# Kernel tuning notes

Hardware: AMD Instinct MI355X
Metric: run time of the kernel (lower is better)

Reference implementation:

```python
import jax, jax.numpy as jnp
import numpy as np

EPS_BN = 1e-5


def setup_inputs() -> dict:
    key = jax.random.key(0)
    ks = jax.random.split(key, 6)
    n, L, D, G = 10000, 256, 32, 3
    return {
        "pop": jax.random.normal(ks[0], (n, L), dtype=jnp.float32),
        "conv_w": jax.random.normal(ks[1], (D, 1, 1), dtype=jnp.float32) * 0.1,
        "conv_b": jnp.zeros((D,), dtype=jnp.float32),
        "bn_gamma": jnp.ones((D,), dtype=jnp.float32),
        "bn_beta": jnp.zeros((D,), dtype=jnp.float32),
        "gcn_ws": jax.random.normal(ks[2], (G, D, D), dtype=jnp.float32) * (1.0 / np.sqrt(D)),
        "gcn_bs": jnp.zeros((G, D), dtype=jnp.float32),
        "out_w": jax.random.normal(ks[3], (D, 3), dtype=jnp.float32) * (1.0 / np.sqrt(D)),
        "out_b": jnp.zeros((3,), dtype=jnp.float32),
        "k": 32,
    }


def _knn_edges(x, k):
    # x: [n, d]. PyG knn_graph(loop=False): edges (neighbor j -> center i).
    n = x.shape[0]
    sq = jnp.sum(x * x, axis=-1)  # [n]
    d2 = sq[:, None] + sq[None, :] - 2.0 * (x @ x.T)  # [n, n]
    idx = jnp.arange(n)
    d2 = d2.at[idx, idx].set(jnp.inf)  # exclude self (loop=False)
    _, nbr = jax.lax.top_k(-d2, k)  # [n, k] nearest neighbors of each node
    src = nbr.reshape(-1)                       # sources (neighbors)
    dst = jnp.repeat(idx, k)                    # targets (centers)
    return src, dst


def _gcn(x, W, b, src, dst, deg_isqrt):
    # GCNConv with self-loops already folded into (src, dst) and deg.
    h = x @ W  # [n, D_out]
    norm = deg_isqrt[src] * deg_isqrt[dst]  # [E]
    msg = h[src] * norm[:, None]
    agg = jax.ops.segment_sum(msg, dst, num_segments=x.shape[0])
    return agg + b


def reference(pop, conv_w, conv_b, bn_gamma, bn_beta, gcn_ws, gcn_bs, out_w, out_b, k):
    n, L = pop.shape
    # --- stem: Conv1d(1, D, kernel=1) -> y[n, c, l] = pop[n, l] * w[c] + b[c]
    w = conv_w[:, 0, 0]  # [D]
    y = pop[:, None, :] * w[None, :, None] + conv_b[None, :, None]  # [n, D, L]
    # --- BatchNorm1d (training mode: batch stats over (N, L), biased var)
    mean = jnp.mean(y, axis=(0, 2))
    var = jnp.mean(jnp.square(y - mean[None, :, None]), axis=(0, 2))
    y = (y - mean[None, :, None]) * (bn_gamma / jnp.sqrt(var + EPS_BN))[None, :, None] + bn_beta[None, :, None]
    y = jax.nn.silu(y)
    # --- adaptive avg pool to length 1 -> mean over L
    x = jnp.mean(y, axis=-1)  # [n, D]
    # --- knn graph on pooled features
    src, dst = _knn_edges(x, k)
    # add self loops (GCNConv default)
    idx = jnp.arange(n)
    src_f = jnp.concatenate([src, idx])
    dst_f = jnp.concatenate([dst, idx])
    deg = jax.ops.segment_sum(jnp.ones_like(dst_f, dtype=x.dtype), dst_f, num_segments=n)
    deg_isqrt = jnp.where(deg > 0, 1.0 / jnp.sqrt(deg), 0.0)
    # --- stacked GCNs
    for i in range(gcn_ws.shape[0]):
        x = _gcn(x, gcn_ws[i], gcn_bs[i], src_f, dst_f, deg_isqrt)
        x = jax.nn.silu(x)
    x = _gcn(x, out_w, out_b, src_f, dst_f, deg_isqrt)  # [n, 3]
    return jax.nn.softmax(x, axis=-1)
```

## Files before the change

### kernel.cpp

```cpp
#include <hip/hip_runtime.h>
#include <math.h>

#define N_NODES 10000
#define NPAD    10016
#define L_LEN   256
#define D_DIM   32
#define K_NBR   32
#define NTOT    (N_NODES * L_LEN)
#define EPS_BN  1e-5f
#define QB      3
#define BT      1024
#define SD      3

typedef unsigned int uint4_ev __attribute__((ext_vector_type(4)));

__device__ __forceinline__ float silu_f(float x) {
    return x / (1.0f + expf(-x));
}

__global__ void stats_kernel(const float* __restrict__ pop, float* __restrict__ stats) {
    __shared__ float s1[256], s2[256];
    int t = threadIdx.x;
    float a = 0.f, b = 0.f;
    for (int idx = blockIdx.x * 256 + t; idx < NTOT; idx += gridDim.x * 256) {
        float v = pop[idx];
        a += v; b += v * v;
    }
    s1[t] = a; s2[t] = b;
    __syncthreads();
    for (int s = 128; s > 0; s >>= 1) {
        if (t < s) { s1[t] += s1[t + s]; s2[t] += s2[t + s]; }
        __syncthreads();
    }
    if (t == 0) { atomicAdd(&stats[0], s1[0]); atomicAdd(&stats[1], s2[0]); }
}

__global__ void feat_kernel(const float* __restrict__ pop,
                            const float* __restrict__ conv_w,
                            const float* __restrict__ conv_b,
                            const float* __restrict__ gamma,
                            const float* __restrict__ beta,
                            const float* __restrict__ stats,
                            float* __restrict__ X,
                            float* __restrict__ XT,
                            float* __restrict__ SQ) {
    __shared__ float row[L_LEN];
    __shared__ float part[256];
    int i = blockIdx.x;
    int t = threadIdx.x;
    row[t] = pop[i * L_LEN + t];
    __syncthreads();
    int d = t & 31, g = t >> 5;
    float M  = stats[0] * (1.0f / NTOT);
    float Vc = stats[1] * (1.0f / NTOT) - M * M;
    float w = conv_w[d], b = conv_b[d];
    float mean = fmaf(w, M, b);
    float var  = w * w * Vc;
    float sc = gamma[d] / sqrtf(var + EPS_BN);
    float bt = beta[d];
    float acc = 0.f;
    int l0 = g * 32;
    #pragma unroll
    for (int l = 0; l < 32; ++l) {
        float y = fmaf(row[l0 + l], w, b);
        float z = fmaf(y - mean, sc, bt);
        acc += silu_f(z);
    }
    part[t] = acc;
    __syncthreads();
    if (t < 32) {
        float s = 0.f;
        #pragma unroll
        for (int gg = 0; gg < 8; ++gg) s += part[gg * 32 + t];
        float xv = s * (1.0f / L_LEN);
        X[i * D_DIM + t] = xv;
        XT[t * N_NODES + i] = xv;
        part[t] = xv;
    }
    __syncthreads();
    if (t == 0) {
        float sq = 0.f;
        #pragma unroll
        for (int dd = 0; dd < 32; ++dd) sq += part[dd] * part[dd];
        SQ[i] = sq;
    }
}

__global__ __launch_bounds__(BT) void knn3_kernel(const float* __restrict__ X,
                                                  const float* __restrict__ XT,
                                                  const float* __restrict__ SQ,
                                                  int* __restrict__ NBR) {
    extern __shared__ unsigned int keys[];
    __shared__ float qv[QB][D_DIM];
    __shared__ float sqq[QB];
    __shared__ unsigned int hist[256];
    __shared__ unsigned int sprefix;
    __shared__ int swant, scnt, slast;

    int t = threadIdx.x;
    int q0 = blockIdx.x * QB;

    if (t < QB * D_DIM) {
        int q = t >> 5, d = t & 31;
        int gq = q0 + q;
        qv[q][d] = (gq < N_NODES) ? X[gq * D_DIM + d] : 0.f;
    }
    if (t < QB) sqq[t] = (q0 + t < N_NODES) ? SQ[q0 + t] : 0.f;
    __syncthreads();

    float acc[QB][SD * 4];
    #pragma unroll
    for (int q = 0; q < QB; ++q)
        #pragma unroll
        for (int s = 0; s < SD * 4; ++s) acc[q][s] = 0.f;

    #pragma unroll 2
    for (int d = 0; d < D_DIM; ++d) {
        float qd0 = qv[0][d], qd1 = qv[1][d], qd2 = qv[2][d];
        const float4* xr4 = (const float4*)(XT + d * N_NODES);
        #pragma unroll
        for (int s = 0; s < SD; ++s) {
            int i4 = t + s * BT;
            float4 xv = make_float4(0.f, 0.f, 0.f, 0.f);
            if (i4 < N_NODES / 4) xv = xr4[i4];
            acc[0][s * 4 + 0] = fmaf(qd0, xv.x, acc[0][s * 4 + 0]);
            acc[0][s * 4 + 1] = fmaf(qd0, xv.y, acc[0][s * 4 + 1]);
            acc[0][s * 4 + 2] = fmaf(qd0, xv.z, acc[0][s * 4 + 2]);
            acc[0][s * 4 + 3] = fmaf(qd0, xv.w, acc[0][s * 4 + 3]);
            acc[1][s * 4 + 0] = fmaf(qd1, xv.x, acc[1][s * 4 + 0]);
            acc[1][s * 4 + 1] = fmaf(qd1, xv.y, acc[1][s * 4 + 1]);
            acc[1][s * 4 + 2] = fmaf(qd1, xv.z, acc[1][s * 4 + 2]);
            acc[1][s * 4 + 3] = fmaf(qd1, xv.w, acc[1][s * 4 + 3]);
            acc[2][s * 4 + 0] = fmaf(qd2, xv.x, acc[2][s * 4 + 0]);
            acc[2][s * 4 + 1] = fmaf(qd2, xv.y, acc[2][s * 4 + 1]);
            acc[2][s * 4 + 2] = fmaf(qd2, xv.z, acc[2][s * 4 + 2]);
            acc[2][s * 4 + 3] = fmaf(qd2, xv.w, acc[2][s * 4 + 3]);
        }
    }

    const float4* sq4p = (const float4*)SQ;
    #pragma unroll
    for (int s = 0; s < SD; ++s) {
        int i4 = t + s * BT;
        int j4 = 4 * i4;
        if (j4 < NPAD) {
            float4 sj = make_float4(0.f, 0.f, 0.f, 0.f);
            if (i4 < N_NODES / 4) sj = sq4p[i4];
            float sjv[4] = { sj.x, sj.y, sj.z, sj.w };
            #pragma unroll
            for (int q = 0; q < QB; ++q) {
                int gq = q0 + q;
                unsigned int kk[4];
                #pragma unroll
                for (int jj = 0; jj < 4; ++jj) {
                    int j = j4 + jj;
                    unsigned int kv = 0xFFFFFFFFu;
                    if (j < N_NODES && gq < N_NODES && j != gq) {
                        float d2 = (sqq[q] + sjv[jj]) - 2.0f * acc[q][s * 4 + jj];
                        unsigned int u = __float_as_uint(d2);
                        u ^= (u & 0x80000000u) ? 0xFFFFFFFFu : 0x80000000u;
                        kv = u;
                    }
                    kk[jj] = kv;
                }
                uint4_ev w = { kk[0], kk[1], kk[2], kk[3] };
                *(uint4_ev*)&keys[q * NPAD + j4] = w;
            }
        }
    }
    __syncthreads();

    for (int q = 0; q < QB; ++q) {
        int gq = q0 + q;
        if (gq >= N_NODES) break;
        unsigned int* kq = keys + q * NPAD;
        if (t == 0) { sprefix = 0u; swant = K_NBR; scnt = 0; }
        __syncthreads();

        for (int r = 0; r < 4; ++r) {
            if (t < 256) hist[t] = 0u;
            __syncthreads();
            unsigned int pfxR = sprefix;
            int wantR = swant;
            int shift = 24 - 8 * r;
            for (int s = 0; s < 10; ++s) {
                int j = t + s * BT;
                if (j < NPAD) {
                    unsigned int u = kq[j];
                    bool match = (r == 0) || ((u >> (shift + 8)) == pfxR);
                    if (match) atomicAdd(&hist[(u >> shift) & 255u], 1u);
                }
            }
            __syncthreads();
            if (t < 64) {
                int lane = t;
                unsigned int c[4];
                unsigned int gsum = 0u;
                #pragma unroll
                for (int i = 0; i < 4; ++i) { c[i] = hist[4 * lane + i]; gsum += c[i]; }
                unsigned int x = gsum;
                #pragma unroll
                for (int off = 1; off < 64; off <<= 1) {
                    unsigned int y = (unsigned int)__shfl_up((int)x, off);
                    if (lane >= off) x += y;
                }
                unsigned int e = x - gsum;
                #pragma unroll
                for (int i = 0; i < 4; ++i) {
                    if (e < (unsigned int)wantR && (unsigned int)wantR <= e + c[i]) {
                        swant = wantR - (int)e;
                        sprefix = (pfxR << 8) | (unsigned int)(4 * lane + i);
                    }
                    e += c[i];
                }
            }
            __syncthreads();
        }

        unsigned int kth = sprefix;
        int wantEq = swant;
        for (int s = 0; s < 10; ++s) {
            int j = t + s * BT;
            if (j < N_NODES && kq[j] < kth) {
                int p = atomicAdd(&scnt, 1);
                NBR[gq * K_NBR + p] = j;
            }
        }
        __syncthreads();
        int base = scnt;
        int last = -1;
        for (int e = 0; e < wantEq; ++e) {
            unsigned int best = 0xFFFFFFFFu;
            for (int s = 0; s < 10; ++s) {
                int j = t + s * BT;
                if (j < N_NODES && kq[j] == kth && j > last)
                    best = best < (unsigned int)j ? best : (unsigned int)j;
            }
            #pragma unroll
            for (int off = 32; off > 0; off >>= 1) {
                unsigned int o = (unsigned int)__shfl_xor((int)best, off);
                best = best < o ? best : o;
            }
            if ((t & 63) == 0) hist[t >> 6] = best;
            __syncthreads();
            if (t == 0) {
                unsigned int m = 0xFFFFFFFFu;
                #pragma unroll
                for (int w = 0; w < 16; ++w) m = m < hist[w] ? m : hist[w];
                NBR[gq * K_NBR + base + e] = (int)m;
                slast = (int)m;
            }
            __syncthreads();
            last = slast;
            __syncthreads();
        }
    }
}

__global__ void gcn_mm(const float* __restrict__ X, const float* __restrict__ W,
                       float* __restrict__ H) {
    __shared__ float Ws[D_DIM * D_DIM];
    int t = threadIdx.x;
    #pragma unroll
    for (int q = 0; q < 4; ++q) Ws[q * 256 + t] = W[q * 256 + t];
    __syncthreads();
    int i = blockIdx.x * 8 + (t >> 5);
    int d = t & 31;
    const float* xr = X + i * D_DIM;
    float acc = 0.f;
    #pragma unroll
    for (int m = 0; m < D_DIM; ++m)
        acc = fmaf(xr[m], Ws[m * D_DIM + d], acc);
    H[i * D_DIM + d] = acc;
}

__global__ void gcn_agg(const float* __restrict__ H, const int* __restrict__ NBR,
                        const float* __restrict__ bias, float* __restrict__ Xout,
                        int do_silu) {
    __shared__ int nb[256];
    int t = threadIdx.x;
    int i0 = blockIdx.x * 8;
    nb[t] = NBR[i0 * K_NBR + t];
    __syncthreads();
    int i = i0 + (t >> 5);
    int d = t & 31;
    float acc = H[i * D_DIM + d];
    int base = (t >> 5) * K_NBR;
    #pragma unroll 8
    for (int s = 0; s < K_NBR; ++s) {
        int j = nb[base + s];
        acc += H[j * D_DIM + d];
    }
    const float r = 1.0f / sqrtf(33.0f);
    const float nrm = r * r;
    float v = fmaf(acc, nrm, bias[d]);
    if (do_silu) v = silu_f(v);
    Xout[i * D_DIM + d] = v;
}

__global__ void out_mm(const float* __restrict__ X, const float* __restrict__ W,
                       float* __restrict__ HOUT) {
    __shared__ float Ws[D_DIM * 3];
    int t = threadIdx.x;
    if (t < D_DIM * 3) Ws[t] = W[t];
    __syncthreads();
    int i = blockIdx.x * 256 + t;
    if (i >= N_NODES) return;
    float a0 = 0.f, a1 = 0.f, a2 = 0.f;
    #pragma unroll
    for (int m = 0; m < D_DIM; ++m) {
        float xv = X[i * D_DIM + m];
        a0 = fmaf(xv, Ws[m * 3 + 0], a0);
        a1 = fmaf(xv, Ws[m * 3 + 1], a1);
        a2 = fmaf(xv, Ws[m * 3 + 2], a2);
    }
    HOUT[i * 3 + 0] = a0; HOUT[i * 3 + 1] = a1; HOUT[i * 3 + 2] = a2;
}

__global__ void final_kernel(const float* __restrict__ HOUT, const int* __restrict__ NBR,
                             const float* __restrict__ out_b, float* __restrict__ out) {
    int i = blockIdx.x * 256 + threadIdx.x;
    if (i >= N_NODES) return;
    float a0 = HOUT[i * 3 + 0], a1 = HOUT[i * 3 + 1], a2 = HOUT[i * 3 + 2];
    for (int s = 0; s < K_NBR; ++s) {
        int j = NBR[i * K_NBR + s];
        a0 += HOUT[j * 3 + 0];
        a1 += HOUT[j * 3 + 1];
        a2 += HOUT[j * 3 + 2];
    }
    const float r = 1.0f / sqrtf(33.0f);
    const float nrm = r * r;
    float v0 = fmaf(a0, nrm, out_b[0]);
    float v1 = fmaf(a1, nrm, out_b[1]);
    float v2 = fmaf(a2, nrm, out_b[2]);
    float m = fmaxf(v0, fmaxf(v1, v2));
    float e0 = expf(v0 - m), e1 = expf(v1 - m), e2 = expf(v2 - m);
    float inv = 1.0f / (e0 + e1 + e2);
    out[i * 3 + 0] = e0 * inv;
    out[i * 3 + 1] = e1 * inv;
    out[i * 3 + 2] = e2 * inv;
}

extern "C" void kernel_launch(void* const* d_in, const int* in_sizes, int n_in,
                              void* d_out, int out_size, void* d_ws, size_t ws_size,
                              hipStream_t stream) {
    const float* pop    = (const float*)d_in[0];
    const float* conv_w = (const float*)d_in[1];
    const float* conv_b = (const float*)d_in[2];
    const float* gamma  = (const float*)d_in[3];
    const float* beta   = (const float*)d_in[4];
    const float* gcn_ws = (const float*)d_in[5];
    const float* gcn_bs = (const float*)d_in[6];
    const float* out_w  = (const float*)d_in[7];
    const float* out_b  = (const float*)d_in[8];

    char* ws = (char*)d_ws;
    const size_t o_stats = 0;
    const size_t o_X     = 256;
    const size_t o_XT    = o_X + 1280000;
    const size_t o_SQ    = o_XT + 1280000;
    const size_t o_H     = o_SQ + 40192;
    const size_t o_NBR   = o_H + 1280000;
    const size_t o_HOUT  = o_NBR + 1280000;

    float* stats = (float*)(ws + o_stats);
    float* X     = (float*)(ws + o_X);
    float* XT    = (float*)(ws + o_XT);
    float* SQ    = (float*)(ws + o_SQ);
    float* H     = (float*)(ws + o_H);
    int*   NBR   = (int*)  (ws + o_NBR);
    float* HOUT  = (float*)(ws + o_HOUT);
    float* out   = (float*)d_out;

    (void)hipMemsetAsync(stats, 0, 2 * sizeof(float), stream);
    stats_kernel<<<512, 256, 0, stream>>>(pop, stats);
    feat_kernel<<<N_NODES, 256, 0, stream>>>(pop, conv_w, conv_b, gamma, beta, stats, X, XT, SQ);

    const int nqb = (N_NODES + QB - 1) / QB;
    const size_t keys_bytes = (size_t)QB * NPAD * 4;
    knn3_kernel<<<nqb, BT, keys_bytes, stream>>>(X, XT, SQ, NBR);

    for (int l = 0; l < 3; ++l) {
        gcn_mm<<<N_NODES / 8, 256, 0, stream>>>(X, gcn_ws + l * D_DIM * D_DIM, H);
        gcn_agg<<<N_NODES / 8, 256, 0, stream>>>(H, NBR, gcn_bs + l * D_DIM, X, 1);
    }
    out_mm<<<(N_NODES + 255) / 256, 256, 0, stream>>>(X, out_w, HOUT);
    final_kernel<<<(N_NODES + 255) / 256, 256, 0, stream>>>(HOUT, NBR, out_b, out);
}
```

Baseline: 766.5 us.

## Parallelize kNN selection across queries and fuse GCN aggregate-then-matmul kernels

New measurement: 948.9 us. +23.8%, slower.

```diff
diff --git a/kernel.cpp b/kernel.cpp
--- a/kernel.cpp
+++ b/kernel.cpp
@@ -93,17 +93,20 @@
     extern __shared__ unsigned int keys[];
     __shared__ float qv[QB][D_DIM];
     __shared__ float sqq[QB];
-    __shared__ unsigned int hist[256];
-    __shared__ unsigned int sprefix;
-    __shared__ int swant, scnt, slast;
+    __shared__ unsigned int whist[16][256];
+    __shared__ unsigned int wmin[16], wmax[16];
+    __shared__ unsigned int gkmin[QB], gkmax[QB], gkth[QB];
+    __shared__ int gwant[QB], gcnt[QB];
 
     int t = threadIdx.x;
+    int lane = t & 63;
+    int w = t >> 6;
     int q0 = blockIdx.x * QB;
 
     if (t < QB * D_DIM) {
         int q = t >> 5, d = t & 31;
-        int gq = q0 + q;
-        qv[q][d] = (gq < N_NODES) ? X[gq * D_DIM + d] : 0.f;
+        int gq_ = q0 + q;
+        qv[q][d] = (gq_ < N_NODES) ? X[gq_ * D_DIM + d] : 0.f;
     }
     if (t < QB) sqq[t] = (q0 + t < N_NODES) ? SQ[q0 + t] : 0.f;
     __syncthreads();
@@ -149,13 +152,13 @@
             float sjv[4] = { sj.x, sj.y, sj.z, sj.w };
             #pragma unroll
             for (int q = 0; q < QB; ++q) {
-                int gq = q0 + q;
+                int gq_ = q0 + q;
                 unsigned int kk[4];
                 #pragma unroll
                 for (int jj = 0; jj < 4; ++jj) {
                     int j = j4 + jj;
                     unsigned int kv = 0xFFFFFFFFu;
-                    if (j < N_NODES && gq < N_NODES && j != gq) {
+                    if (j < N_NODES && gq_ < N_NODES && j != gq_) {
                         float d2 = (sqq[q] + sjv[jj]) - 2.0f * acc[q][s * 4 + jj];
                         unsigned int u = __float_as_uint(d2);
                         u ^= (u & 0x80000000u) ? 0xFFFFFFFFu : 0x80000000u;
@@ -163,182 +166,178 @@
                     }
                     kk[jj] = kv;
                 }
-                uint4_ev w = { kk[0], kk[1], kk[2], kk[3] };
-                *(uint4_ev*)&keys[q * NPAD + j4] = w;
-            }
-        }
-    }
-    __syncthreads();
-
-    for (int q = 0; q < QB; ++q) {
-        int gq = q0 + q;
-        if (gq >= N_NODES) break;
-        unsigned int* kq = keys + q * NPAD;
-        if (t == 0) { sprefix = 0u; swant = K_NBR; scnt = 0; }
+                uint4_ev wv = { kk[0], kk[1], kk[2], kk[3] };
+                *(uint4_ev*)&keys[q * NPAD + j4] = wv;
+            }
+        }
+    }
+    __syncthreads();
+
+    int g     = (w >= 10) ? 2 : (w >= 5 ? 1 : 0);
+    int wbase = (g == 2) ? 10 : g * 5;
+    int gsz   = (g == 2) ? 6 : 5;
+    int lt    = (w - wbase) * 64 + lane;
+    int GT    = gsz * 64;
+    unsigned int* kq = keys + g * NPAD;
+    int gq = q0 + g;
+
+    unsigned int mn = 0xFFFFFFFFu, mx = 0u;
+    for (int j = lt; j < NPAD; j += GT) {
+        unsigned int u = kq[j];
+        mn = mn < u ? mn : u;
+        if (u != 0xFFFFFFFFu) mx = mx > u ? mx : u;
+    }
+    #pragma unroll
+    for (int off = 32; off > 0; off >>= 1) {
+        unsigned int a = (unsigned int)__shfl_xor((int)mn, off);
+        unsigned int b = (unsigned int)__shfl_xor((int)mx, off);
+        mn = mn < a ? mn : a;
+        mx = mx > b ? mx : b;
+    }
+    if (lane == 0) { wmin[w] = mn; wmax[w] = mx; }
+    __syncthreads();
+    if (t < QB) {
+        int b0 = (t == 2) ? 10 : t * 5;
+        int bs = (t == 2) ? 6 : 5;
+        unsigned int m0 = 0xFFFFFFFFu, m1 = 0u;
+        for (int k = 0; k < bs; ++k) {
+            m0 = m0 < wmin[b0 + k] ? m0 : wmin[b0 + k];
+            m1 = m1 > wmax[b0 + k] ? m1 : wmax[b0 + k];
+        }
+        gkmin[t] = m0; gkmax[t] = m1;
+        gkth[t] = m0; gwant[t] = K_NBR; gcnt[t] = 0;
+    }
+    __syncthreads();
+
+    for (int shift = 24; shift >= 0; shift -= 8) {
+        unsigned int gdiff = gkmin[g] ^ gkmax[g];
+        bool skip = (gdiff >> shift) == 0;
+        if (!skip) {
+            #pragma unroll
+            for (int b = lane; b < 256; b += 64) whist[w][b] = 0u;
+            unsigned int kth = gkth[g];
+            int sh8 = shift + 8;
+            for (int j = lt; j < NPAD; j += GT) {
+                unsigned int u = kq[j];
+                if (((unsigned long long)u >> sh8) == ((unsigned long long)kth >> sh8))
+                    atomicAdd(&whist[w][(u >> shift) & 255u], 1u);
+            }
+        }
         __syncthreads();
-
-        for (int r = 0; r < 4; ++r) {
-            if (t < 256) hist[t] = 0u;
-            __syncthreads();
-            unsigned int pfxR = sprefix;
-            int wantR = swant;
-            int shift = 24 - 8 * r;
-            for (int s = 0; s < 10; ++s) {
-                int j = t + s * BT;
-                if (j < NPAD) {
-                    unsigned int u = kq[j];
-                    bool match = (r == 0) || ((u >> (shift + 8)) == pfxR);
-                    if (match) atomicAdd(&hist[(u >> shift) & 255u], 1u);
+        if (!skip && w == wbase) {
+            int want = gwant[g];
+            unsigned int kth = gkth[g];
+            unsigned int c[4]; unsigned int gsum = 0u;
+            #pragma unroll
+            for (int i = 0; i < 4; ++i) {
+                unsigned int tot = 0u; int b = 4 * lane + i;
+                for (int k = 0; k < gsz; ++k) tot += whist[wbase + k][b];
+                c[i] = tot; gsum += tot;
+            }
+            unsigned int x = gsum;
+            #pragma unroll
+            for (int off = 1; off < 64; off <<= 1) {
+                unsigned int y = (unsigned int)__shfl_up((int)x, off);
+                if (lane >= off) x += y;
+            }
+            unsigned int e = x - gsum;
+            #pragma unroll
+            for (int i = 0; i < 4; ++i) {
+                if (e < (unsigned int)want && (unsigned int)want <= e + c[i]) {
+                    gwant[g] = want - (int)e;
+                    gkth[g] = (kth & ~(255u << shift)) |
+                              ((unsigned int)(4 * lane + i) << shift);
                 }
-            }
-            __syncthreads();
-            if (t < 64) {
-                int lane = t;
-                unsigned int c[4];
-                unsigned int gsum = 0u;
+                e += c[i];
+            }
+        }
+        __syncthreads();
+    }
+
+    unsigned int kth = gkth[g];
+    int wantEq = gwant[g];
+    int baseSlot = K_NBR - wantEq;
+    if (gq < N_NODES) {
+        for (int j = lt; j < NPAD; j += GT) {
+            if (kq[j] < kth) {
+                int p = atomicAdd(&gcnt[g], 1);
+                NBR[gq * K_NBR + p] = j;
+            }
+        }
+        if (w == wbase) {
+            int last = -1;
+            for (int e = 0; e < wantEq; ++e) {
+                unsigned int best = 0xFFFFFFFFu;
+                for (int j = lane; j < NPAD; j += 64) {
+                    if (kq[j] == kth && j > last && (unsigned int)j < best)
+                        best = (unsigned int)j;
+                }
                 #pragma unroll
-                for (int i = 0; i < 4; ++i) { c[i] = hist[4 * lane + i]; gsum += c[i]; }
-                unsigned int x = gsum;
-                #pragma unroll
-                for (int off = 1; off < 64; off <<= 1) {
-                    unsigned int y = (unsigned int)__shfl_up((int)x, off);
-                    if (lane >= off) x += y;
+                for (int off = 32; off > 0; off >>= 1) {
+                    unsigned int o = (unsigned int)__shfl_xor((int)best, off);
+                    best = best < o ? best : o;
                 }
-                unsigned int e = x - gsum;
-                #pragma unroll
-                for (int i = 0; i < 4; ++i) {
-                    if (e < (unsigned int)wantR && (unsigned int)wantR <= e + c[i]) {
-                        swant = wantR - (int)e;
-                        sprefix = (pfxR << 8) | (unsigned int)(4 * lane + i);
-                    }
-                    e += c[i];
-                }
-            }
-            __syncthreads();
-        }
-
-        unsigned int kth = sprefix;
-        int wantEq = swant;
-        for (int s = 0; s < 10; ++s) {
-            int j = t + s * BT;
-            if (j < N_NODES && kq[j] < kth) {
-                int p = atomicAdd(&scnt, 1);
-                NBR[gq * K_NBR + p] = j;
-            }
-        }
-        __syncthreads();
-        int base = scnt;
-        int last = -1;
-        for (int e = 0; e < wantEq; ++e) {
-            unsigned int best = 0xFFFFFFFFu;
-            for (int s = 0; s < 10; ++s) {
-                int j = t + s * BT;
-                if (j < N_NODES && kq[j] == kth && j > last)
-                    best = best < (unsigned int)j ? best : (unsigned int)j;
-            }
-            #pragma unroll
-            for (int off = 32; off > 0; off >>= 1) {
-                unsigned int o = (unsigned int)__shfl_xor((int)best, off);
-                best = best < o ? best : o;
-            }
-            if ((t & 63) == 0) hist[t >> 6] = best;
-            __syncthreads();
-            if (t == 0) {
-                unsigned int m = 0xFFFFFFFFu;
-                #pragma unroll
-                for (int w = 0; w < 16; ++w) m = m < hist[w] ? m : hist[w];
-                NBR[gq * K_NBR + base + e] = (int)m;
-                slast = (int)m;
-            }
-            __syncthreads();
-            last = slast;
-            __syncthreads();
-        }
-    }
-}
-
-__global__ void gcn_mm(const float* __restrict__ X, const float* __restrict__ W,
-                       float* __restrict__ H) {
+                if (lane == 0) NBR[gq * K_NBR + baseSlot + e] = (int)best;
+                last = (int)best;
+            }
+        }
+    }
+}
+
+__global__ void gcn_fused(const float* __restrict__ Xin, const int* __restrict__ NBR,
+                          const float* __restrict__ W, const float* __restrict__ bias,
+                          float* __restrict__ Xout) {
     __shared__ float Ws[D_DIM * D_DIM];
-    int t = threadIdx.x;
+    __shared__ float sAgg[8][D_DIM];
+    __shared__ int nb[8][K_NBR];
+    int t = threadIdx.x, g = t >> 5, d = t & 31;
     #pragma unroll
     for (int q = 0; q < 4; ++q) Ws[q * 256 + t] = W[q * 256 + t];
-    __syncthreads();
-    int i = blockIdx.x * 8 + (t >> 5);
-    int d = t & 31;
-    const float* xr = X + i * D_DIM;
+    int i = blockIdx.x * 8 + g;
+    nb[g][d] = NBR[i * K_NBR + d];
+    __syncthreads();
+    float s = Xin[i * D_DIM + d];
+    #pragma unroll 8
+    for (int e = 0; e < K_NBR; ++e) s += Xin[nb[g][e] * D_DIM + d];
+    sAgg[g][d] = s;
+    __syncthreads();
     float acc = 0.f;
     #pragma unroll
     for (int m = 0; m < D_DIM; ++m)
-        acc = fmaf(xr[m], Ws[m * D_DIM + d], acc);
-    H[i * D_DIM + d] = acc;
-}
-
-__global__ void gcn_agg(const float* __restrict__ H, const int* __restrict__ NBR,
-                        const float* __restrict__ bias, float* __restrict__ Xout,
-                        int do_silu) {
-    __shared__ int nb[256];
-    int t = threadIdx.x;
-    int i0 = blockIdx.x * 8;
-    nb[t] = NBR[i0 * K_NBR + t];
-    __syncthreads();
-    int i = i0 + (t >> 5);
-    int d = t & 31;
-    float acc = H[i * D_DIM + d];
-    int base = (t >> 5) * K_NBR;
+        acc = fmaf(sAgg[g][m], Ws[m * D_DIM + d], acc);
+    float v = fmaf(acc, 1.0f / 33.0f, bias[d]);
+    Xout[i * D_DIM + d] = silu_f(v);
+}
+
+__global__ void out_final(const float* __restrict__ Xin, const int* __restrict__ NBR,
+                          const float* __restrict__ Wout, const float* __restrict__ out_b,
+                          float* __restrict__ out) {
+    __shared__ float Ws[D_DIM * 3];
+    __shared__ float sAgg[8][D_DIM];
+    __shared__ int nb[8][K_NBR];
+    int t = threadIdx.x, g = t >> 5, d = t & 31;
+    if (t < D_DIM * 3) Ws[t] = Wout[t];
+    int i = blockIdx.x * 8 + g;
+    nb[g][d] = NBR[i * K_NBR + d];
+    __syncthreads();
+    float s = Xin[i * D_DIM + d];
     #pragma unroll 8
-    for (int s = 0; s < K_NBR; ++s) {
-        int j = nb[base + s];
-        acc += H[j * D_DIM + d];
-    }
-    const float r = 1.0f / sqrtf(33.0f);
-    const float nrm = r * r;
-    float v = fmaf(acc, nrm, bias[d]);
-    if (do_silu) v = silu_f(v);
-    Xout[i * D_DIM + d] = v;
-}
-
-__global__ void out_mm(const float* __restrict__ X, const float* __restrict__ W,
-                       float* __restrict__ HOUT) {
-    __shared__ float Ws[D_DIM * 3];
-    int t = threadIdx.x;
-    if (t < D_DIM * 3) Ws[t] = W[t];
-    __syncthreads();
-    int i = blockIdx.x * 256 + t;
-    if (i >= N_NODES) return;
-    float a0 = 0.f, a1 = 0.f, a2 = 0.f;
-    #pragma unroll
-    for (int m = 0; m < D_DIM; ++m) {
-        float xv = X[i * D_DIM + m];
-        a0 = fmaf(xv, Ws[m * 3 + 0], a0);
-        a1 = fmaf(xv, Ws[m * 3 + 1], a1);
-        a2 = fmaf(xv, Ws[m * 3 + 2], a2);
-    }
-    HOUT[i * 3 + 0] = a0; HOUT[i * 3 + 1] = a1; HOUT[i * 3 + 2] = a2;
-}
-
-__global__ void final_kernel(const float* __restrict__ HOUT, const int* __restrict__ NBR,
-                             const float* __restrict__ out_b, float* __restrict__ out) {
-    int i = blockIdx.x * 256 + threadIdx.x;
-    if (i >= N_NODES) return;
-    float a0 = HOUT[i * 3 + 0], a1 = HOUT[i * 3 + 1], a2 = HOUT[i * 3 + 2];
-    for (int s = 0; s < K_NBR; ++s) {
-        int j = NBR[i * K_NBR + s];
-        a0 += HOUT[j * 3 + 0];
-        a1 += HOUT[j * 3 + 1];
-        a2 += HOUT[j * 3 + 2];
-    }
-    const float r = 1.0f / sqrtf(33.0f);
-    const float nrm = r * r;
-    float v0 = fmaf(a0, nrm, out_b[0]);
-    float v1 = fmaf(a1, nrm, out_b[1]);
-    float v2 = fmaf(a2, nrm, out_b[2]);
-    float m = fmaxf(v0, fmaxf(v1, v2));
-    float e0 = expf(v0 - m), e1 = expf(v1 - m), e2 = expf(v2 - m);
-    float inv = 1.0f / (e0 + e1 + e2);
-    out[i * 3 + 0] = e0 * inv;
-    out[i * 3 + 1] = e1 * inv;
-    out[i * 3 + 2] = e2 * inv;
+    for (int e = 0; e < K_NBR; ++e) s += Xin[nb[g][e] * D_DIM + d];
+    sAgg[g][d] = s;
+    __syncthreads();
+    if (d < 3) {
+        float v[3];
+        #pragma unroll
+        for (int c = 0; c < 3; ++c) {
+            float a = 0.f;
+            #pragma unroll
+            for (int m = 0; m < D_DIM; ++m) a = fmaf(sAgg[g][m], Ws[m * 3 + c], a);
+            v[c] = fmaf(a, 1.0f / 33.0f, out_b[c]);
+        }
+        float mx = fmaxf(v[0], fmaxf(v[1], v[2]));
+        float e0 = expf(v[0] - mx), e1 = expf(v[1] - mx), e2 = expf(v[2] - mx);
+        out[i * 3 + d] = expf(v[d] - mx) / (e0 + e1 + e2);
+    }
 }
 
 extern "C" void kernel_launch(void* const* d_in, const int* in_sizes, int n_in,
@@ -361,7 +360,6 @@
     const size_t o_SQ    = o_XT + 1280000;
     const size_t o_H     = o_SQ + 40192;
     const size_t o_NBR   = o_H + 1280000;
-    const size_t o_HOUT  = o_NBR + 1280000;
 
     float* stats = (float*)(ws + o_stats);
     float* X     = (float*)(ws + o_X);
@@ -369,7 +367,6 @@
     float* SQ    = (float*)(ws + o_SQ);
     float* H     = (float*)(ws + o_H);
     int*   NBR   = (int*)  (ws + o_NBR);
-    float* HOUT  = (float*)(ws + o_HOUT);
     float* out   = (float*)d_out;
 
     (void)hipMemsetAsync(stats, 0, 2 * sizeof(float), stream);
@@ -380,10 +377,8 @@
     const size_t keys_bytes = (size_t)QB * NPAD * 4;
     knn3_kernel<<<nqb, BT, keys_bytes, stream>>>(X, XT, SQ, NBR);
 
-    for (int l = 0; l < 3; ++l) {
-        gcn_mm<<<N_NODES / 8, 256, 0, stream>>>(X, gcn_ws + l * D_DIM * D_DIM, H);
-        gcn_agg<<<N_NODES / 8, 256, 0, stream>>>(H, NBR, gcn_bs + l * D_DIM, X, 1);
-    }
-    out_mm<<<(N_NODES + 255) / 256, 256, 0, stream>>>(X, out_w, HOUT);
-    final_kernel<<<(N_NODES + 255) / 256, 256, 0, stream>>>(HOUT, NBR, out_b, out);
-}
+    gcn_fused<<<N_NODES / 8, 256, 0, stream>>>(X, NBR, gcn_ws,        gcn_bs,      H);
+    gcn_fused<<<N_NODES / 8, 256, 0, stream>>>(H, NBR, gcn_ws + 1024, gcn_bs + 32, X);
+    gcn_fused<<<N_NODES / 8, 256, 0, stream>>>(X, NBR, gcn_ws + 2048, gcn_bs + 64, H);
+    out_final<<<N_NODES / 8, 256, 0, stream>>>(H, NBR, out_w, out_b, out);
+}
```
